# Kernel tuning notes

Measured on AMD Instinct MI355X. Metric: run time of the kernel, lower is better.

## Reference

```python
import jax, jax.numpy as jnp
import numpy as np


def setup_inputs() -> dict:
    key = jax.random.key(0)
    k1, k2 = jax.random.split(key)
    B, T, D = 16, 512, 384
    MAX_LEN = 4096
    x = jax.random.normal(k1, (B, T, D), dtype=jnp.float32)
    durations = jax.random.randint(k2, (B, T), 0, 8, dtype=jnp.int64)
    return {"x": x, "durations": durations, "max_len": MAX_LEN}


def reference(x, durations, max_len):
    # x: (B, T, D), durations: (B, T) int
    B, T, D = x.shape
    cum = jnp.cumsum(durations, axis=1)          # (B, T) exclusive-of-nothing cumulative ends
    mel_len = cum[:, -1]                         # (B,) actual (uncapped) frame lengths
    frames = jnp.arange(max_len)                 # (F,)
    # phoneme index owning each output frame: searchsorted on cumulative ends
    idx = jax.vmap(lambda c: jnp.searchsorted(c, frames, side='right'))(cum)  # (B, F)
    idx = jnp.clip(idx, 0, T - 1)
    out = jnp.take_along_axis(x, idx[:, :, None], axis=1)  # (B, F, D)
    # zero-pad frames beyond each item's length (and beyond max_len truncation)
    valid = frames[None, :] < jnp.minimum(mel_len, max_len)[:, None]  # (B, F)
    out = out * valid[:, :, None].astype(out.dtype)
    return out, mel_len
```

## Files before the change

kernel.cpp:

```cpp
#include <hip/hip_runtime.h>


#define B_ 16
#define T_ 512
#define D_ 384
#define MAXLEN_ 4096
#define ROWV4_ (D_ / 4)
#define OUT_ELEMS_ (B_ * MAXLEN_ * D_)
#define BLOCKS_PER_BATCH_ ((MAXLEN_ * ROWV4_) / 256)

__global__ __launch_bounds__(T_) void lr_scan_kernel(const int* __restrict__ dur,
                                                     int* __restrict__ cum_ws,
                                                     float* __restrict__ mel_out) {
    const int b = blockIdx.x, t = threadIdx.x;
    const int lane = t & 63, w = t >> 6;
    int v = dur[b * T_ + t];
    #pragma unroll
    for (int off = 1; off < 64; off <<= 1) {
        int n = __shfl_up(v, off);
        if (lane >= off) v += n;
    }
    __shared__ int wsum[8];
    if (lane == 63) wsum[w] = v;
    __syncthreads();
    if (t < 8) {
        int u = wsum[t];
        #pragma unroll
        for (int off = 1; off < 8; off <<= 1) {
            int n = __shfl_up(u, off);
            if (t >= off) u += n;
        }
        wsum[t] = u;
    }
    __syncthreads();
    const int cum = v + (w > 0 ? wsum[w - 1] : 0);
    cum_ws[b * T_ + t] = cum;
    if (t == T_ - 1) mel_out[b] = (float)cum;
}

__global__ __launch_bounds__(256) void lr_gather_kernel(const float4* __restrict__ x,
                                                        const int* __restrict__ cum_ws,
                                                        const int* __restrict__ max_len_p,
                                                        float4* __restrict__ out) {
    __shared__ int s[T_];
    const int t = threadIdx.x;
    const int b = blockIdx.x / BLOCKS_PER_BATCH_;
    const int* cb = cum_ws + b * T_;
    s[t] = cb[t];
    s[t + 256] = cb[t + 256];
    __syncthreads();

    const int g = blockIdx.x * 256 + t;
    const int row = g / ROWV4_;
    const int col = g - row * ROWV4_;
    const int f = row & (MAXLEN_ - 1);
    const int mel = s[T_ - 1];
    const int max_len = max_len_p[0];

    float4 v = make_float4(0.f, 0.f, 0.f, 0.f);
    if (f < mel && f < max_len) {
        int idx = 0;
        #pragma unroll
        for (int step = 256; step > 0; step >>= 1)
            if (s[idx + step - 1] <= f) idx += step;
        if (idx > T_ - 1) idx = T_ - 1;
        v = x[(b * T_ + idx) * ROWV4_ + col];
    }
    out[g] = v;
}

extern "C" void kernel_launch(void* const* d_in, const int* in_sizes, int n_in,
                              void* d_out, int out_size, void* d_ws, size_t ws_size,
                              hipStream_t stream) {
    const float* x = (const float*)d_in[0];
    const int* dur = (const int*)d_in[1];
    const int* max_len_p = (const int*)d_in[2];

    float* out = (float*)d_out;
    float* mel_out = out + OUT_ELEMS_;
    int* cum_ws = (int*)d_ws;

    lr_scan_kernel<<<B_, T_, 0, stream>>>(dur, cum_ws, mel_out);

    const int total_v4 = OUT_ELEMS_ / 4;
    lr_gather_kernel<<<total_v4 / 256, 256, 0, stream>>>(
        (const float4*)x, cum_ws, max_len_p, (float4*)out);
}
```

Baseline: 122.3 us.

## Fuse duration scan into gather kernel with larger blocks and nontemporal stores

Removes the separate scan kernel and its workspace round-trip: each 1024-thread gather block now recomputes the prefix sum of its batch's durations in shared memory before doing the binary search and gather. Block size grows from 256 to 1024 so the redundant scan is spread over more output elements, and output writes use nontemporal stores to avoid polluting cache with the large write-only stream. The cost is redundant scan work in every block, two extra barriers, and larger blocks that may reduce scheduling flexibility.

```diff
diff --git a/kernel.cpp b/kernel.cpp
--- a/kernel.cpp
+++ b/kernel.cpp
@@ -7,21 +7,33 @@
 #define MAXLEN_ 4096
 #define ROWV4_ (D_ / 4)
 #define OUT_ELEMS_ (B_ * MAXLEN_ * D_)
-#define BLOCKS_PER_BATCH_ ((MAXLEN_ * ROWV4_) / 256)
+#define BLK_ 1024
+#define BLOCKS_PER_BATCH_ ((MAXLEN_ * ROWV4_) / BLK_)
+#define GRID_ (B_ * BLOCKS_PER_BATCH_)
 
-__global__ __launch_bounds__(T_) void lr_scan_kernel(const int* __restrict__ dur,
-                                                     int* __restrict__ cum_ws,
-                                                     float* __restrict__ mel_out) {
-    const int b = blockIdx.x, t = threadIdx.x;
+typedef float v4f __attribute__((ext_vector_type(4)));
+
+__global__ __launch_bounds__(BLK_) void lr_fused_kernel(const v4f* __restrict__ x,
+                                                        const int* __restrict__ dur,
+                                                        const int* __restrict__ max_len_p,
+                                                        v4f* __restrict__ out,
+                                                        float* __restrict__ mel_out) {
+    __shared__ int s[T_];
+    __shared__ int wsum[8];
+    const int t = threadIdx.x;
+    const int b = blockIdx.x / BLOCKS_PER_BATCH_;
+
+    int v = 0;
     const int lane = t & 63, w = t >> 6;
-    int v = dur[b * T_ + t];
-    #pragma unroll
-    for (int off = 1; off < 64; off <<= 1) {
-        int n = __shfl_up(v, off);
-        if (lane >= off) v += n;
+    if (t < T_) {
+        v = dur[b * T_ + t];
+        #pragma unroll
+        for (int off = 1; off < 64; off <<= 1) {
+            int n = __shfl_up(v, off);
+            if (lane >= off) v += n;
+        }
+        if (lane == 63) wsum[w] = v;
     }
-    __shared__ int wsum[8];
-    if (lane == 63) wsum[w] = v;
     __syncthreads();
     if (t < 8) {
         int u = wsum[t];
@@ -33,40 +45,29 @@
         wsum[t] = u;
     }
     __syncthreads();
-    const int cum = v + (w > 0 ? wsum[w - 1] : 0);
-    cum_ws[b * T_ + t] = cum;
-    if (t == T_ - 1) mel_out[b] = (float)cum;
-}
-
-__global__ __launch_bounds__(256) void lr_gather_kernel(const float4* __restrict__ x,
-                                                        const int* __restrict__ cum_ws,
-                                                        const int* __restrict__ max_len_p,
-                                                        float4* __restrict__ out) {
-    __shared__ int s[T_];
-    const int t = threadIdx.x;
-    const int b = blockIdx.x / BLOCKS_PER_BATCH_;
-    const int* cb = cum_ws + b * T_;
-    s[t] = cb[t];
-    s[t + 256] = cb[t + 256];
+    if (t < T_) s[t] = v + (w > 0 ? wsum[w - 1] : 0);
     __syncthreads();
 
-    const int g = blockIdx.x * 256 + t;
+    const int g = blockIdx.x * BLK_ + t;
     const int row = g / ROWV4_;
     const int col = g - row * ROWV4_;
     const int f = row & (MAXLEN_ - 1);
     const int mel = s[T_ - 1];
     const int max_len = max_len_p[0];
 
-    float4 v = make_float4(0.f, 0.f, 0.f, 0.f);
+    v4f ov = (v4f){0.f, 0.f, 0.f, 0.f};
     if (f < mel && f < max_len) {
         int idx = 0;
         #pragma unroll
         for (int step = 256; step > 0; step >>= 1)
             if (s[idx + step - 1] <= f) idx += step;
         if (idx > T_ - 1) idx = T_ - 1;
-        v = x[(b * T_ + idx) * ROWV4_ + col];
+        ov = x[(b * T_ + idx) * ROWV4_ + col];
     }
-    out[g] = v;
+    __builtin_nontemporal_store(ov, &out[g]);
+
+    if (t == 0 && (blockIdx.x % BLOCKS_PER_BATCH_) == 0)
+        mel_out[b] = (float)mel;
 }
 
 extern "C" void kernel_launch(void* const* d_in, const int* in_sizes, int n_in,
@@ -78,11 +79,8 @@
 
     float* out = (float*)d_out;
     float* mel_out = out + OUT_ELEMS_;
-    int* cum_ws = (int*)d_ws;
+    (void)d_ws; (void)ws_size;
 
-    lr_scan_kernel<<<B_, T_, 0, stream>>>(dur, cum_ws, mel_out);
-
-    const int total_v4 = OUT_ELEMS_ / 4;
-    lr_gather_kernel<<<total_v4 / 256, 256, 0, stream>>>(
-        (const float4*)x, cum_ws, max_len_p, (float4*)out);
+    lr_fused_kernel<<<GRID_, BLK_, 0, stream>>>(
+        (const v4f*)x, dur, max_len_p, (v4f*)out, mel_out);
 }
```

New measurement: 129.3 us. +5.7%, slower.
